# Performance work log

Measured on AMD Instinct MI355X. Metric: run time of the kernel, lower is better.

## Reference

```python
import jax, jax.numpy as jnp
import numpy as np


def binarize_weight(W):
    # per-output-channel scale: mean of |W| over all dims except dim 0
    alpha = jnp.mean(jnp.abs(W), axis=tuple(range(1, W.ndim)), keepdims=True)
    return alpha * jnp.sign(W)


def setup_inputs() -> dict:
    key = jax.random.key(0)
    k1, k2, k3 = jax.random.split(key, 3)
    B, S, D_IN, D_OUT = 4, 2048, 4096, 4096
    x = jax.random.normal(k1, (B, S, D_IN), dtype=jnp.float32)
    weight_real = jax.random.normal(k2, (D_OUT, D_IN), dtype=jnp.float32)
    bias = jax.random.normal(k3, (D_OUT,), dtype=jnp.float32)
    return {"x": x, "weight_real": weight_real, "bias": bias}


def reference(x, weight_real, bias):
    W = binarize_weight(weight_real)          # [out, in]
    # F.linear: x @ W.T + b
    return jnp.einsum("bsi,oi->bso", x, W) + bias
```

## Files before the change

kernel.cpp:

```cpp
#include <hip/hip_runtime.h>
#include <hip/hip_bf16.h>
#include <stdint.h>

typedef __bf16 bf16x8_t __attribute__((ext_vector_type(8)));
typedef float f32x4 __attribute__((ext_vector_type(4)));
typedef int i32x4 __attribute__((ext_vector_type(4)));

__device__ __forceinline__ unsigned short f2bf_rne(float f) {
  unsigned int u = __float_as_uint(f);
  u += 0x7FFFu + ((u >> 16) & 1u);
  return (unsigned short)(u >> 16);
}

__global__ __launch_bounds__(256) void k_prep_w_i8(const float* __restrict__ W,
                                                   signed char* __restrict__ wq,
                                                   float* __restrict__ alpha, int K) {
  const int o = blockIdx.x;
  const float* row = W + (size_t)o * K;
  signed char* orow = wq + (size_t)o * K;
  const int tid = threadIdx.x;
  float s = 0.f;
  const int nj = K / 1024;
  for (int j = 0; j < nj; ++j) {
    int base = j * 1024 + tid * 4;
    float4 v = *reinterpret_cast<const float4*>(row + base);
    s += fabsf(v.x) + fabsf(v.y) + fabsf(v.z) + fabsf(v.w);
    char4 sg;
    sg.x = v.x > 0.f ? 1 : (v.x < 0.f ? -1 : 0);
    sg.y = v.y > 0.f ? 1 : (v.y < 0.f ? -1 : 0);
    sg.z = v.z > 0.f ? 1 : (v.z < 0.f ? -1 : 0);
    sg.w = v.w > 0.f ? 1 : (v.w < 0.f ? -1 : 0);
    *reinterpret_cast<char4*>(orow + base) = sg;
  }
  for (int off = 32; off > 0; off >>= 1) s += __shfl_down(s, off);
  __shared__ float red[4];
  int lane = tid & 63, wid = tid >> 6;
  if (lane == 0) red[wid] = s;
  __syncthreads();
  if (tid == 0) alpha[o] = (red[0] + red[1] + red[2] + red[3]) / (float)K;
}

__global__ __launch_bounds__(256) void k_quant_x(const float* __restrict__ x,
                                                 signed char* __restrict__ xq,
                                                 float* __restrict__ srw, int K) {
  const int m = blockIdx.x;
  const float* row = x + (size_t)m * K;
  signed char* orow = xq + (size_t)m * K;
  const int tid = threadIdx.x;
  const int nj = K / 1024;
  float mx = 0.f;
  for (int j = 0; j < nj; ++j) {
    int base = j * 1024 + tid * 4;
    float4 v = *reinterpret_cast<const float4*>(row + base);
    mx = fmaxf(mx, fmaxf(fmaxf(fabsf(v.x), fabsf(v.y)), fmaxf(fabsf(v.z), fabsf(v.w))));
  }
  for (int off = 32; off > 0; off >>= 1) mx = fmaxf(mx, __shfl_down(mx, off));
  __shared__ float red[4];
  int lane = tid & 63, wid = tid >> 6;
  if (lane == 0) red[wid] = mx;
  __syncthreads();
  mx = fmaxf(fmaxf(red[0], red[1]), fmaxf(red[2], red[3]));
  const float inv_s = (mx > 0.f) ? (127.f / mx) : 0.f;
  if (tid == 0) srw[m] = mx * (1.f / 127.f);
  for (int j = 0; j < nj; ++j) {
    int base = j * 1024 + tid * 4;
    float4 v = *reinterpret_cast<const float4*>(row + base);
    char4 q;
    q.x = (signed char)__float2int_rn(v.x * inv_s);
    q.y = (signed char)__float2int_rn(v.y * inv_s);
    q.z = (signed char)__float2int_rn(v.z * inv_s);
    q.w = (signed char)__float2int_rn(v.w * inv_s);
    *reinterpret_cast<char4*>(orow + base) = q;
  }
}

__global__ __launch_bounds__(256) void k_prep_w(const float* __restrict__ W,
                                                unsigned short* __restrict__ wb,
                                                float* __restrict__ alpha, int K) {
  const int o = blockIdx.x;
  const float* row = W + (size_t)o * K;
  unsigned short* orow = wb + (size_t)o * K;
  const int tid = threadIdx.x;
  float s = 0.f;
  const int nj = K / 1024;
  for (int j = 0; j < nj; ++j) {
    int base = j * 1024 + tid * 4;
    float4 v = *reinterpret_cast<const float4*>(row + base);
    s += fabsf(v.x) + fabsf(v.y) + fabsf(v.z) + fabsf(v.w);
    ushort4 sg;
    sg.x = v.x > 0.f ? 0x3F80u : (v.x < 0.f ? 0xBF80u : 0u);
    sg.y = v.y > 0.f ? 0x3F80u : (v.y < 0.f ? 0xBF80u : 0u);
    sg.z = v.z > 0.f ? 0x3F80u : (v.z < 0.f ? 0xBF80u : 0u);
    sg.w = v.w > 0.f ? 0x3F80u : (v.w < 0.f ? 0xBF80u : 0u);
    *reinterpret_cast<ushort4*>(orow + base) = sg;
  }
  for (int off = 32; off > 0; off >>= 1) s += __shfl_down(s, off);
  __shared__ float red[4];
  int lane = tid & 63, wid = tid >> 6;
  if (lane == 0) red[wid] = s;
  __syncthreads();
  if (tid == 0) alpha[o] = (red[0] + red[1] + red[2] + red[3]) / (float)K;
}

__global__ __launch_bounds__(256) void k_conv_x(const float* __restrict__ x,
                                                unsigned short* __restrict__ xb,
                                                long long n4) {
  long long i = (long long)blockIdx.x * blockDim.x + threadIdx.x;
  const long long stride = (long long)gridDim.x * blockDim.x;
  for (; i < n4; i += stride) {
    float4 v = reinterpret_cast<const float4*>(x)[i];
    ushort4 o;
    o.x = f2bf_rne(v.x);
    o.y = f2bf_rne(v.y);
    o.z = f2bf_rne(v.z);
    o.w = f2bf_rne(v.w);
    reinterpret_cast<ushort4*>(xb)[i] = o;
  }
}

#define GLDS(gp, lp)                                                                   \
  __builtin_amdgcn_global_load_lds((const __attribute__((address_space(1))) void*)(gp),\
                                   (__attribute__((address_space(3))) void*)(lp), 16, 0, 0)

__global__ __launch_bounds__(512, 2) void k_gemm256_i8(
    const signed char* __restrict__ A, const signed char* __restrict__ B,
    const float* __restrict__ alpha, const float* __restrict__ bias,
    const float* __restrict__ srw, float* __restrict__ C,
    int M, int N, int K, int tm, int tn) {
  __shared__ __attribute__((aligned(128))) signed char lds[131072];

  const int nwg = tm * tn;
  const int chunk = nwg >> 3;
  int mT, nT;
  {
    const int bid = blockIdx.x;
    const int mPC = (tn > 0 && chunk % tn == 0) ? (chunk / tn) : 0;
    if ((nwg & 7) == 0 && mPC > 0 && (tm % mPC) == 0) {
      const int c = bid & 7;
      const int q = bid >> 3;
      mT = c * mPC + (q % mPC);
      nT = q / mPC;
    } else {
      mT = bid % tm;
      nT = bid / tm;
    }
  }
  const long m0 = (long)mT * 256;
  const int n0 = nT * 256;

  const int tid = threadIdx.x;
  const int lane = tid & 63;
  const int w = tid >> 6;
  const int wr = w >> 2;
  const int wc = w & 3;
  const int lr = lane & 15;
  const int l16 = lane >> 4;

  const int sgr = (w << 4) + (lane >> 2);
  const int gsl = lane & 3;
  const signed char* gA = A + (size_t)(m0 + sgr) * K + gsl * 16;
  const signed char* gB = B + (size_t)(n0 + sgr) * K + gsl * 16;
  const size_t K128 = (size_t)128 * K;
  signed char* const dst0 = lds + (w << 10);

#define STG_TILE(t_, BB)                          \
  do {                                            \
    const signed char* a_ = gA + (t_) * 64;       \
    const signed char* b_ = gB + (t_) * 64;       \
    GLDS(a_, dst0 + (BB));                        \
    GLDS(a_ + K128, dst0 + (BB) + 8192);          \
    GLDS(b_, dst0 + (BB) + 16384);                \
    GLDS(b_ + K128, dst0 + (BB) + 24576);         \
  } while (0)
#define FRAGI(off) (*reinterpret_cast<const i32x4*>(&lds[off]))
#define BAR __builtin_amdgcn_s_barrier()
#define SCHED0 __builtin_amdgcn_sched_barrier(0)

  const int pA = (wr * 128 + lr) * 64 + (l16 << 4);
  const int pB = 16384 + (wc * 64 + lr) * 64 + (l16 << 4);

  i32x4 acc[8][4];
#pragma unroll
  for (int i = 0; i < 8; ++i)
#pragma unroll
    for (int j = 0; j < 4; ++j) acc[i][j] = (i32x4){0, 0, 0, 0};

  const int NT = K >> 6;

  auto tile = [&](int T, int BB) {
    SCHED0;
    if (T + 2 < NT) {
      asm volatile("s_waitcnt vmcnt(8)" ::: "memory");
    } else if (T + 1 < NT) {
      asm volatile("s_waitcnt vmcnt(4)" ::: "memory");
    } else {
      asm volatile("s_waitcnt vmcnt(0)" ::: "memory");
    }
    BAR;
    SCHED0;
    i32x4 aF[8], bF[4];
#pragma unroll
    for (int j = 0; j < 4; ++j) bF[j] = FRAGI(BB + pB + j * 1024);
#pragma unroll
    for (int i = 0; i < 8; ++i) aF[i] = FRAGI(BB + pA + i * 1024);
    if (T + 3 < NT) STG_TILE(T + 3, ((T + 3) & 3) * 32768);
#pragma unroll
    for (int i = 0; i < 8; ++i)
#pragma unroll
      for (int j = 0; j < 4; ++j)
        acc[i][j] = __builtin_amdgcn_mfma_i32_16x16x64_i8(aF[i], bF[j], acc[i][j], 0, 0, 0);
  };

  STG_TILE(0, 0);
  STG_TILE(1, 32768);
  STG_TILE(2, 65536);

  for (int T = 0; T < NT; T += 4) {
    tile(T, 0);
    tile(T + 1, 32768);
    tile(T + 2, 65536);
    tile(T + 3, 98304);
  }

  float4 sr[8];
#pragma unroll
  for (int i = 0; i < 8; ++i) {
    const long row = m0 + wr * 128 + i * 16 + l16 * 4;
    sr[i] = *reinterpret_cast<const float4*>(&srw[row]);
  }
#pragma unroll
  for (int j = 0; j < 4; ++j) {
    const int col = n0 + wc * 64 + j * 16 + lr;
    const float al = alpha[col];
    const float bi = bias[col];
#pragma unroll
    for (int i = 0; i < 8; ++i) {
      const long row = m0 + wr * 128 + i * 16 + l16 * 4;
      i32x4 v = acc[i][j];
      C[(size_t)(row + 0) * N + col] = (float)v[0] * sr[i].x * al + bi;
      C[(size_t)(row + 1) * N + col] = (float)v[1] * sr[i].y * al + bi;
      C[(size_t)(row + 2) * N + col] = (float)v[2] * sr[i].z * al + bi;
      C[(size_t)(row + 3) * N + col] = (float)v[3] * sr[i].w * al + bi;
    }
  }
#undef STG_TILE
#undef FRAGI
#undef BAR
#undef SCHED0
}

__global__ __launch_bounds__(256) void k_gemm(
    const unsigned short* __restrict__ A, const unsigned short* __restrict__ B,
    const float* __restrict__ alpha, const float* __restrict__ bias,
    float* __restrict__ C, int M, int N, int K, int tm) {
  __shared__ unsigned short tA[128 * 32];
  __shared__ unsigned short tB[128 * 32];
  const int bid = blockIdx.x;
  const int mT = bid % tm;
  const int nT = bid / tm;
  const int m0 = mT * 128, n0 = nT * 128;
  const int tid = threadIdx.x;
  const int lane = tid & 63;
  const int wid = tid >> 6;
  const int wr = wid >> 1, wc = wid & 1;
  f32x4 acc[4][4];
#pragma unroll
  for (int i = 0; i < 4; ++i)
#pragma unroll
    for (int j = 0; j < 4; ++j) acc[i][j] = (f32x4){0.f, 0.f, 0.f, 0.f};
  const int srow = wid * 16 + (lane >> 2);
  const int scol = (lane & 3) * 8;
  const unsigned short* gA0 = A + (size_t)(m0 + srow) * K + scol;
  const unsigned short* gA1 = A + (size_t)(m0 + 64 + srow) * K + scol;
  const unsigned short* gB0 = B + (size_t)(n0 + srow) * K + scol;
  const unsigned short* gB1 = B + (size_t)(n0 + 64 + srow) * K + scol;
  unsigned short* lA0 = tA + wid * 512;
  unsigned short* lA1 = tA + 2048 + wid * 512;
  unsigned short* lB0 = tB + wid * 512;
  unsigned short* lB1 = tB + 2048 + wid * 512;
  const int lr = lane & 15;
  const int kb = lane >> 4;
  int aoff[4], boff[4];
#pragma unroll
  for (int i = 0; i < 4; ++i) {
    aoff[i] = (wr * 64 + i * 16 + lr) * 32 + kb * 8;
    boff[i] = (wc * 64 + i * 16 + lr) * 32 + kb * 8;
  }
  for (int k0 = 0; k0 < K; k0 += 32) {
    __syncthreads();
    GLDS(gA0 + k0, lA0);
    GLDS(gA1 + k0, lA1);
    GLDS(gB0 + k0, lB0);
    GLDS(gB1 + k0, lB1);
    __syncthreads();
    bf16x8_t af[4], bfr[4];
#pragma unroll
    for (int i = 0; i < 4; ++i) af[i] = *reinterpret_cast<const bf16x8_t*>(&tA[aoff[i]]);
#pragma unroll
    for (int j = 0; j < 4; ++j) bfr[j] = *reinterpret_cast<const bf16x8_t*>(&tB[boff[j]]);
#pragma unroll
    for (int i = 0; i < 4; ++i)
#pragma unroll
      for (int j = 0; j < 4; ++j)
        acc[i][j] = __builtin_amdgcn_mfma_f32_16x16x32_bf16(af[i], bfr[j], acc[i][j], 0, 0, 0);
  }
#pragma unroll
  for (int j = 0; j < 4; ++j) {
    const int col = n0 + wc * 64 + j * 16 + lr;
    const float al = alpha[col];
    const float bi = bias[col];
#pragma unroll
    for (int i = 0; i < 4; ++i) {
      const int row = m0 + wr * 64 + i * 16 + kb * 4;
      f32x4 v = acc[i][j];
#pragma unroll
      for (int r = 0; r < 4; ++r) C[(size_t)(row + r) * N + col] = v[r] * al + bi;
    }
  }
}

__global__ void k_naive(const float* __restrict__ x, const float* __restrict__ W,
                        const float* __restrict__ bias, float* __restrict__ out,
                        int M, int N, int K) {
  int m = blockIdx.x;
  int n = blockIdx.y * 256 + threadIdx.x;
  if (n >= N) return;
  const float* xr = x + (size_t)m * K;
  const float* wr = W + (size_t)n * K;
  float sa = 0.f, s = 0.f;
  for (int i = 0; i < K; ++i) {
    float wv = wr[i];
    sa += fabsf(wv);
    float sg = (wv > 0.f) ? 1.f : ((wv < 0.f) ? -1.f : 0.f);
    s += xr[i] * sg;
  }
  out[(size_t)m * N + n] = (sa / (float)K) * s + bias[n];
}

extern "C" void kernel_launch(void* const* d_in, const int* in_sizes, int n_in,
                              void* d_out, int out_size, void* d_ws, size_t ws_size,
                              hipStream_t stream) {
  const float* x = (const float*)d_in[0];
  const float* w = (const float*)d_in[1];
  const float* bias = (const float*)d_in[2];
  float* out = (float*)d_out;

  const int D_OUT = in_sizes[2];
  const int D_IN = in_sizes[1] / D_OUT;
  const long long M = (long long)in_sizes[0] / D_IN;
  const int N = D_OUT, K = D_IN;

  const size_t xqB = (size_t)M * K;
  const size_t wqB = (size_t)N * K;
  const size_t need_i8 = xqB + wqB + (size_t)N * 4 + (size_t)M * 4;
  const size_t xbB = (size_t)M * K * 2;
  const size_t wbB = (size_t)N * K * 2;
  const size_t need_bf = xbB + wbB + (size_t)N * 4;

  const bool kok = (K % 1024 == 0);
  const bool f256 = kok && (ws_size >= need_i8) && (M % 256 == 0) && (N % 256 == 0) &&
                    (K % 256 == 0);
  const bool f128 = kok && (ws_size >= need_bf) && (M % 128 == 0) && (N % 128 == 0) &&
                    (K % 32 == 0);

  if (f256) {
    signed char* xq = (signed char*)d_ws;
    signed char* wq = (signed char*)d_ws + xqB;
    float* alpha = (float*)((char*)d_ws + xqB + wqB);
    float* srow = alpha + N;
    k_prep_w_i8<<<N, 256, 0, stream>>>(w, wq, alpha, K);
    k_quant_x<<<(unsigned)M, 256, 0, stream>>>(x, xq, srow, K);
    const int tm = (int)(M / 256), tn = N / 256;
    k_gemm256_i8<<<tm * tn, 512, 0, stream>>>(xq, wq, alpha, bias, srow, out,
                                              (int)M, N, K, tm, tn);
  } else if (f128) {
    unsigned short* xb = (unsigned short*)d_ws;
    unsigned short* wb = (unsigned short*)((char*)d_ws + xbB);
    float* alpha = (float*)((char*)d_ws + xbB + wbB);
    k_prep_w<<<N, 256, 0, stream>>>(w, wb, alpha, K);
    long long n4 = M * (long long)K / 4;
    k_conv_x<<<2048, 256, 0, stream>>>(x, xb, n4);
    const int tm = (int)(M / 128), tn = N / 128;
    k_gemm<<<tm * tn, 256, 0, stream>>>(xb, wb, alpha, bias, out, (int)M, N, K, tm);
  } else {
    dim3 g((unsigned)M, (unsigned)((N + 255) / 256));
    k_naive<<<g, 256, 0, stream>>>(x, w, bias, out, (int)M, N, K);
  }
}
```

Before: 203.4 us.

## Swizzle int8 GEMM LDS layout and cache x rows in registers during quantization

The int8 GEMM now XOR-swizzles the 16-byte chunk position within each 64-byte LDS row, both when staging from global memory and when reading fragments, to reduce LDS bank conflicts on fragment loads. The x quantization kernel keeps the row's float4 values in registers between the max-reduction pass and the quantize pass, so it reads x from global memory once instead of twice. Both changes must agree on the swizzle mapping, and the register cache adds register pressure to the quantize kernel.

```diff
diff --git a/kernel.cpp b/kernel.cpp
--- a/kernel.cpp
+++ b/kernel.cpp
@@ -48,29 +48,50 @@
   signed char* orow = xq + (size_t)m * K;
   const int tid = threadIdx.x;
   const int nj = K / 1024;
-  float mx = 0.f;
-  for (int j = 0; j < nj; ++j) {
-    int base = j * 1024 + tid * 4;
-    float4 v = *reinterpret_cast<const float4*>(row + base);
-    mx = fmaxf(mx, fmaxf(fmaxf(fabsf(v.x), fabsf(v.y)), fmaxf(fabsf(v.z), fabsf(v.w))));
-  }
-  for (int off = 32; off > 0; off >>= 1) mx = fmaxf(mx, __shfl_down(mx, off));
   __shared__ float red[4];
   int lane = tid & 63, wid = tid >> 6;
-  if (lane == 0) red[wid] = mx;
-  __syncthreads();
-  mx = fmaxf(fmaxf(red[0], red[1]), fmaxf(red[2], red[3]));
-  const float inv_s = (mx > 0.f) ? (127.f / mx) : 0.f;
-  if (tid == 0) srw[m] = mx * (1.f / 127.f);
-  for (int j = 0; j < nj; ++j) {
-    int base = j * 1024 + tid * 4;
-    float4 v = *reinterpret_cast<const float4*>(row + base);
-    char4 q;
-    q.x = (signed char)__float2int_rn(v.x * inv_s);
-    q.y = (signed char)__float2int_rn(v.y * inv_s);
-    q.z = (signed char)__float2int_rn(v.z * inv_s);
-    q.w = (signed char)__float2int_rn(v.w * inv_s);
-    *reinterpret_cast<char4*>(orow + base) = q;
+  float mx = 0.f;
+  if (nj <= 8) {
+    float4 rv[8];
+    for (int j = 0; j < nj; ++j) {
+      rv[j] = *reinterpret_cast<const float4*>(row + j * 1024 + tid * 4);
+      mx = fmaxf(mx, fmaxf(fmaxf(fabsf(rv[j].x), fabsf(rv[j].y)),
+                           fmaxf(fabsf(rv[j].z), fabsf(rv[j].w))));
+    }
+    for (int off = 32; off > 0; off >>= 1) mx = fmaxf(mx, __shfl_down(mx, off));
+    if (lane == 0) red[wid] = mx;
+    __syncthreads();
+    mx = fmaxf(fmaxf(red[0], red[1]), fmaxf(red[2], red[3]));
+    const float inv_s = (mx > 0.f) ? (127.f / mx) : 0.f;
+    if (tid == 0) srw[m] = mx * (1.f / 127.f);
+    for (int j = 0; j < nj; ++j) {
+      char4 q;
+      q.x = (signed char)__float2int_rn(rv[j].x * inv_s);
+      q.y = (signed char)__float2int_rn(rv[j].y * inv_s);
+      q.z = (signed char)__float2int_rn(rv[j].z * inv_s);
+      q.w = (signed char)__float2int_rn(rv[j].w * inv_s);
+      *reinterpret_cast<char4*>(orow + j * 1024 + tid * 4) = q;
+    }
+  } else {
+    for (int j = 0; j < nj; ++j) {
+      float4 v = *reinterpret_cast<const float4*>(row + j * 1024 + tid * 4);
+      mx = fmaxf(mx, fmaxf(fmaxf(fabsf(v.x), fabsf(v.y)), fmaxf(fabsf(v.z), fabsf(v.w))));
+    }
+    for (int off = 32; off > 0; off >>= 1) mx = fmaxf(mx, __shfl_down(mx, off));
+    if (lane == 0) red[wid] = mx;
+    __syncthreads();
+    mx = fmaxf(fmaxf(red[0], red[1]), fmaxf(red[2], red[3]));
+    const float inv_s = (mx > 0.f) ? (127.f / mx) : 0.f;
+    if (tid == 0) srw[m] = mx * (1.f / 127.f);
+    for (int j = 0; j < nj; ++j) {
+      float4 v = *reinterpret_cast<const float4*>(row + j * 1024 + tid * 4);
+      char4 q;
+      q.x = (signed char)__float2int_rn(v.x * inv_s);
+      q.y = (signed char)__float2int_rn(v.y * inv_s);
+      q.z = (signed char)__float2int_rn(v.z * inv_s);
+      q.w = (signed char)__float2int_rn(v.w * inv_s);
+      *reinterpret_cast<char4*>(orow + j * 1024 + tid * 4) = q;
+    }
   }
 }
 
@@ -157,7 +178,7 @@
   const int l16 = lane >> 4;
 
   const int sgr = (w << 4) + (lane >> 2);
-  const int gsl = lane & 3;
+  const int gsl = (lane & 3) ^ ((lane >> 3) & 3);
   const signed char* gA = A + (size_t)(m0 + sgr) * K + gsl * 16;
   const signed char* gB = B + (size_t)(n0 + sgr) * K + gsl * 16;
   const size_t K128 = (size_t)128 * K;
@@ -176,8 +197,9 @@
 #define BAR __builtin_amdgcn_s_barrier()
 #define SCHED0 __builtin_amdgcn_sched_barrier(0)
 
-  const int pA = (wr * 128 + lr) * 64 + (l16 << 4);
-  const int pB = 16384 + (wc * 64 + lr) * 64 + (l16 << 4);
+  const int sx = (lr >> 1) & 3;
+  const int pA = (wr * 128 + lr) * 64 + ((l16 ^ sx) << 4);
+  const int pB = 16384 + (wc * 64 + lr) * 64 + ((l16 ^ sx) << 4);
 
   i32x4 acc[8][4];
 #pragma unroll
```

Result: slower. 228.2 us (+12.2%).
